# Kernel optimization log

Measured on AMD Instinct MI355X. Metric: run time of the kernel, lower is better.

The kernel has to match this reference:

```python
import jax, jax.numpy as jnp
import numpy as np

N_NODES = 40000
N_EDGES = 640000
D = 128
N_CLASSES = 40
N_GRAPHS = 128


def setup_inputs() -> dict:
    key = jax.random.key(0)
    ks = jax.random.split(key, 8)
    feat = jax.random.normal(ks[0], (N_NODES, D), dtype=jnp.float32)
    s = 1.0 / np.sqrt(D)
    W1 = jax.random.normal(ks[1], (D, D), dtype=jnp.float32) * s
    b1 = jnp.zeros((D,), dtype=jnp.float32)
    W2 = jax.random.normal(ks[2], (D, D), dtype=jnp.float32) * s
    b2 = jnp.zeros((D,), dtype=jnp.float32)
    Wc = jax.random.normal(ks[3], (D, N_CLASSES), dtype=jnp.float32) * s
    bc = jnp.zeros((N_CLASSES,), dtype=jnp.float32)
    src = jax.random.randint(ks[4], (N_EDGES,), 0, N_NODES, dtype=jnp.int32)
    dst = jax.random.randint(ks[5], (N_EDGES,), 0, N_NODES, dtype=jnp.int32)
    graph_ids = jnp.sort(jax.random.randint(ks[6], (N_ODES := N_NODES,), 0, N_GRAPHS, dtype=jnp.int32))
    return {"feat": feat, "W1": W1, "b1": b1, "W2": W2, "b2": b2,
            "Wc": Wc, "bc": bc, "src": src, "dst": dst, "graph_ids": graph_ids}


def _graph_conv(h, W, b, src, dst, norm_src, norm_dst):
    # DGL GraphConv, norm='both': D_in^{-1/2} A D_out^{-1/2} (h W) + b
    h = (h * norm_src[:, None]) @ W                      # [N, D_out]
    agg = jax.ops.segment_sum(h[src], dst, num_segments=N_NODES)  # SpMM gather-scatter
    return agg * norm_dst[:, None] + b


def reference(feat, W1, b1, W2, b2, Wc, bc, src, dst, graph_ids):
    ones_e = jnp.ones((N_EDGES,), dtype=jnp.float32)
    deg_out = jax.ops.segment_sum(ones_e, src, num_segments=N_NODES)
    deg_in = jax.ops.segment_sum(ones_e, dst, num_segments=N_NODES)
    norm_src = jnp.clip(deg_out, 1.0) ** -0.5
    norm_dst = jnp.clip(deg_in, 1.0) ** -0.5

    h = jax.nn.relu(_graph_conv(feat, W1, b1, src, dst, norm_src, norm_dst))
    h = _graph_conv(h, W2, b2, src, dst, norm_src, norm_dst)

    # dgl.mean_nodes: per-graph mean of node features
    sums = jax.ops.segment_sum(h, graph_ids, num_segments=N_GRAPHS)   # [G, D]
    cnts = jax.ops.segment_sum(jnp.ones((N_NODES,), jnp.float32), graph_ids,
                               num_segments=N_GRAPHS)
    hg = sums / jnp.clip(cnts, 1.0)[:, None]
    return hg @ Wc + bc
```

## Files before the change

kernel.cpp:

```cpp
#include <hip/hip_runtime.h>
#include <hip/hip_fp16.h>

#define N_NODES   40000
#define N_EDGES   640000
#define D         128
#define N_CLASSES 40
#define N_GRAPHS  128

#define SCAN_CHUNK 2048
#define SCAN_NB    ((N_NODES + SCAN_CHUNK - 1) / SCAN_CHUNK)

#define NB_H    128
#define CHUNK_H (N_EDGES / NB_H)
#define NWORDS  (N_NODES / 2)
#define DS_NB   ((NWORDS + 255) / 256)

#define SP2_NPW   5

typedef unsigned int uint;
typedef unsigned short u16;
typedef _Float16 f16x8 __attribute__((ext_vector_type(8)));
typedef float f32x4 __attribute__((ext_vector_type(4)));

__global__ __launch_bounds__(1024) void k_histfuse(const int* __restrict__ src,
                                                   const int* __restrict__ dst,
                                                   uint* __restrict__ cntS,
                                                   uint* __restrict__ cntD,
                                                   const float* __restrict__ W2,
                                                   const float* __restrict__ b2,
                                                   const float* __restrict__ Wc,
                                                   float* __restrict__ Wfused,
                                                   float* __restrict__ bfused,
                                                   float* __restrict__ sums,
                                                   uint* __restrict__ blksum) {
    __shared__ uint h[NWORDS];
    const int bg = blockIdx.x, t = threadIdx.x;
    if (bg >= 2 * NB_H) {
        const int k = bg - 2 * NB_H;
        if (k < N_GRAPHS && t < D) sums[k * D + t] = 0.f;
        if (k == 0 && t < 32) blksum[t] = 0;
        if (t < N_CLASSES) {
            const float* row = (k < D) ? &W2[k * D] : b2;
            float s = 0.f;
            #pragma unroll 8
            for (int j = 0; j < D; ++j) s += row[j] * Wc[j * N_CLASSES + t];
            if (k < D) Wfused[k * N_CLASSES + t] = s;
            else bfused[t] = s;
        }
        return;
    }
    const int b = (bg < NB_H) ? bg : bg - NB_H;
    const int* __restrict__ idx = (bg < NB_H) ? src : dst;
    uint* __restrict__ cnt = (bg < NB_H) ? cntS : cntD;
    for (int i = t; i < NWORDS; i += 1024) h[i] = 0;
    __syncthreads();
    const int base = b * CHUNK_H;
    for (int e = t; e < CHUNK_H; e += 1024) {
        int v = idx[base + e];
        atomicAdd(&h[v >> 1], 1u << ((v & 1) * 16));
    }
    __syncthreads();
    for (int i = t; i < NWORDS; i += 1024) cnt[(size_t)b * NWORDS + i] = h[i];
}

__global__ __launch_bounds__(256) void k_degsum(const uint* __restrict__ cntS,
                                                const uint* __restrict__ cntD,
                                                uint* __restrict__ deg_out,
                                                uint* __restrict__ deg_in,
                                                uint* __restrict__ blksum) {
    __shared__ uint wsum[4];
    const int t = threadIdx.x;
    const int w = blockIdx.x * 256 + t;
    uint tot = 0;
    if (w < NWORDS) {
        uint s0 = 0, s1 = 0, d0 = 0, d1 = 0;
        for (int bb = 0; bb < NB_H; ++bb) {
            uint cs = cntS[(size_t)bb * NWORDS + w];
            s0 += cs & 0xffffu; s1 += cs >> 16;
        }
        for (int bb = 0; bb < NB_H; ++bb) {
            uint cd = cntD[(size_t)bb * NWORDS + w];
            d0 += cd & 0xffffu; d1 += cd >> 16;
        }
        deg_out[2 * w] = s0; deg_out[2 * w + 1] = s1;
        deg_in[2 * w]  = d0; deg_in[2 * w + 1]  = d1;
        tot = d0 + d1;
    }
    #pragma unroll
    for (int off = 32; off > 0; off >>= 1) tot += __shfl_down(tot, off);
    if ((t & 63) == 0) wsum[t >> 6] = tot;
    __syncthreads();
    if (t == 0) atomicAdd(&blksum[blockIdx.x >> 2], wsum[0] + wsum[1] + wsum[2] + wsum[3]);
}

__global__ __launch_bounds__(256, 1) void k_scangemm(const uint* __restrict__ deg_in,
                                                     const uint* __restrict__ blksum,
                                                     uint* __restrict__ offsets,
                                                     const int* __restrict__ gid,
                                                     int* __restrict__ bounds,
                                                     const float* __restrict__ feat,
                                                     const float* __restrict__ W1,
                                                     const uint* __restrict__ deg_out,
                                                     __half* __restrict__ hW) {
    __shared__ uint wsum[4];
    const int t = threadIdx.x;
    if (blockIdx.x < SCAN_NB) {
        const int b = blockIdx.x;
        const int lane = t & 63, wave = t >> 6;
        uint basesum = 0;
        for (int q = 0; q < b; ++q) basesum += blksum[q];
        const int base = b * SCAN_CHUNK + t * 8;
        uint v[8];
        uint s = 0;
        #pragma unroll
        for (int j = 0; j < 8; ++j) {
            int idx = base + j;
            v[j] = (idx < N_NODES) ? deg_in[idx] : 0u;
            s += v[j];
        }
        uint inc = s;
        #pragma unroll
        for (int off = 1; off < 64; off <<= 1) {
            uint o = __shfl_up(inc, off);
            if (lane >= off) inc += o;
        }
        if (lane == 63) wsum[wave] = inc;
        __syncthreads();
        if (t < 4) {
            uint w = wsum[t];
            #pragma unroll
            for (int off = 1; off < 4; off <<= 1) {
                uint o = __shfl_up(w, off);
                if (t >= off) w += o;
            }
            wsum[t] = w;
        }
        __syncthreads();
        uint excl = inc - s + (wave ? wsum[wave - 1] : 0u) + basesum;
        #pragma unroll
        for (int j = 0; j < 8; ++j) {
            int idx = base + j;
            if (idx < N_NODES) offsets[idx] = excl;
            excl += v[j];
        }
        if (b == SCAN_NB - 1 && t == 255) offsets[N_NODES] = excl;
        for (int j = 0; j < 8; ++j) {
            int idx = base + j;
            if (idx >= N_NODES) break;
            int g = gid[idx];
            if (idx == 0) {
                for (int q = 0; q <= g; ++q) bounds[q] = 0;
            } else {
                int gp = gid[idx - 1];
                for (int q = gp + 1; q <= g; ++q) bounds[q] = idx;
            }
            if (idx == N_NODES - 1) {
                for (int q = g + 1; q <= N_GRAPHS; ++q) bounds[q] = N_NODES;
            }
        }
        return;
    }
    const int wv = t >> 6, l = t & 63;
    const int kg = l >> 4;
    const int c  = l & 15;
    const int r0 = (blockIdx.x - SCAN_NB) * 64 + wv * 16;

    f16x8 B[4][8];
    #pragma unroll
    for (int ks = 0; ks < 4; ++ks) {
        #pragma unroll
        for (int nt = 0; nt < 8; ++nt) {
            const int kb = ks * 32 + kg * 8;
            const int col = nt * 16 + c;
            f16x8 b;
            #pragma unroll
            for (int i = 0; i < 8; ++i)
                b[i] = (_Float16)W1[(kb + i) * D + col];
            B[ks][nt] = b;
        }
    }

    f32x4 acc[8];
    #pragma unroll
    for (int nt = 0; nt < 8; ++nt) acc[nt] = (f32x4){0.f, 0.f, 0.f, 0.f};

    const int arow = r0 + c;
    #pragma unroll
    for (int ks = 0; ks < 4; ++ks) {
        const float4 q0 = *(const float4*)&feat[(size_t)arow * D + ks * 32 + kg * 8];
        const float4 q1 = *(const float4*)&feat[(size_t)arow * D + ks * 32 + kg * 8 + 4];
        f16x8 a;
        a[0] = (_Float16)q0.x; a[1] = (_Float16)q0.y;
        a[2] = (_Float16)q0.z; a[3] = (_Float16)q0.w;
        a[4] = (_Float16)q1.x; a[5] = (_Float16)q1.y;
        a[6] = (_Float16)q1.z; a[7] = (_Float16)q1.w;
        #pragma unroll
        for (int nt = 0; nt < 8; ++nt)
            acc[nt] = __builtin_amdgcn_mfma_f32_16x16x32_f16(a, B[ks][nt], acc[nt], 0, 0, 0);
    }

    const int rloc = kg * 4;
    float ns[4];
    #pragma unroll
    for (int r = 0; r < 4; ++r)
        ns[r] = rsqrtf(fmaxf((float)deg_out[r0 + rloc + r], 1.f));
    #pragma unroll
    for (int nt = 0; nt < 8; ++nt) {
        #pragma unroll
        for (int r = 0; r < 4; ++r)
            hW[(size_t)(r0 + rloc + r) * D + nt * 16 + c] =
                __float2half(acc[nt][r] * ns[r]);
    }
}

__global__ void k_base(const uint* __restrict__ cntD, u16* __restrict__ baseDelta) {
    int i = blockIdx.x * blockDim.x + threadIdx.x;
    if (i >= N_NODES) return;
    uint run = 0;
    for (int b = 0; b < NB_H; ++b) {
        baseDelta[(size_t)b * N_NODES + i] = (u16)run;
        run += (cntD[(size_t)b * NWORDS + (i >> 1)] >> ((i & 1) * 16)) & 0xffffu;
    }
}

__global__ __launch_bounds__(1024) void k_place(const int* __restrict__ src,
                                                const int* __restrict__ dst,
                                                const uint* __restrict__ offsets,
                                                const u16* __restrict__ baseDelta,
                                                int* __restrict__ csr) {
    __shared__ uint rk[NWORDS];
    const int b = blockIdx.x, t = threadIdx.x;
    for (int i = t; i < NWORDS; i += 1024) rk[i] = 0;
    __syncthreads();
    const int base = b * CHUNK_H;
    for (int e = t; e < CHUNK_H; e += 1024) {
        int d = dst[base + e];
        uint sh = (d & 1) * 16;
        uint old = atomicAdd(&rk[d >> 1], 1u << sh);
        uint r = (old >> sh) & 0xffffu;
        csr[offsets[d] + baseDelta[(size_t)b * N_NODES + d] + r] = src[base + e];
    }
}

__global__ __launch_bounds__(256) void k_spmm1(const __half* __restrict__ X,
                                               const int* __restrict__ csr_src,
                                               const uint* __restrict__ offsets,
                                               const uint* __restrict__ deg_out,
                                               const uint* __restrict__ deg_in,
                                               const float* __restrict__ b1,
                                               __half2* __restrict__ outp) {
    const int lane = threadIdx.x & 63;
    const __half2* __restrict__ Xr = (const __half2*)X;
    int gw = (blockIdx.x * blockDim.x + threadIdx.x) >> 6;
    int nw = (gridDim.x * blockDim.x) >> 6;
    for (int i = gw; i < N_NODES; i += nw) {
        uint e = offsets[i], e1 = offsets[i + 1];
        float2 acc = {0.f, 0.f};
        for (; e + 4 <= e1; e += 4) {
            int s0 = csr_src[e], s1 = csr_src[e + 1];
            int s2 = csr_src[e + 2], s3 = csr_src[e + 3];
            float2 v0 = __half22float2(Xr[(size_t)s0 * 64 + lane]);
            float2 v1 = __half22float2(Xr[(size_t)s1 * 64 + lane]);
            float2 v2 = __half22float2(Xr[(size_t)s2 * 64 + lane]);
            float2 v3 = __half22float2(Xr[(size_t)s3 * 64 + lane]);
            acc.x += (v0.x + v1.x) + (v2.x + v3.x);
            acc.y += (v0.y + v1.y) + (v2.y + v3.y);
        }
        for (; e < e1; ++e) {
            int s = csr_src[e];
            float2 v = __half22float2(Xr[(size_t)s * 64 + lane]);
            acc.x += v.x; acc.y += v.y;
        }
        float nd = rsqrtf(fmaxf((float)deg_in[i], 1.f));
        float ns = rsqrtf(fmaxf((float)deg_out[i], 1.f));
        float2 b = *(const float2*)&b1[lane * 2];
        float rx = fmaxf(acc.x * nd + b.x, 0.f) * ns;
        float ry = fmaxf(acc.y * nd + b.y, 0.f) * ns;
        outp[(size_t)i * 64 + lane] = __floats2half2_rn(rx, ry);
    }
}

__global__ __launch_bounds__(256) void k_spmm2pool(const __half* __restrict__ X,
                                                   const int* __restrict__ csr_src,
                                                   const uint* __restrict__ offsets,
                                                   const uint* __restrict__ deg_in,
                                                   const int* __restrict__ gid,
                                                   float* __restrict__ sums) {
    const int lane = threadIdx.x & 63;
    const int w = (blockIdx.x * blockDim.x + threadIdx.x) >> 6;
    int n0 = w * SP2_NPW;
    if (n0 >= N_NODES) return;
    int n1 = n0 + SP2_NPW; if (n1 > N_NODES) n1 = N_NODES;
    const __half2* __restrict__ Xr = (const __half2*)X;
    float2 seg = {0.f, 0.f};
    int cur = gid[n0];
    for (int i = n0; i < n1; ++i) {
        int g = gid[i];
        if (g != cur) {
            atomicAdd(&sums[cur * D + 2 * lane], seg.x);
            atomicAdd(&sums[cur * D + 2 * lane + 1], seg.y);
            seg.x = 0.f; seg.y = 0.f; cur = g;
        }
        uint e = offsets[i], e1 = offsets[i + 1];
        float2 acc = {0.f, 0.f};
        for (; e + 4 <= e1; e += 4) {
            int s0 = csr_src[e], s1 = csr_src[e + 1];
            int s2 = csr_src[e + 2], s3 = csr_src[e + 3];
            float2 v0 = __half22float2(Xr[(size_t)s0 * 64 + lane]);
            float2 v1 = __half22float2(Xr[(size_t)s1 * 64 + lane]);
            float2 v2 = __half22float2(Xr[(size_t)s2 * 64 + lane]);
            float2 v3 = __half22float2(Xr[(size_t)s3 * 64 + lane]);
            acc.x += (v0.x + v1.x) + (v2.x + v3.x);
            acc.y += (v0.y + v1.y) + (v2.y + v3.y);
        }
        for (; e < e1; ++e) {
            int s = csr_src[e];
            float2 v = __half22float2(Xr[(size_t)s * 64 + lane]);
            acc.x += v.x; acc.y += v.y;
        }
        float nd = rsqrtf(fmaxf((float)deg_in[i], 1.f));
        seg.x += acc.x * nd;
        seg.y += acc.y * nd;
    }
    atomicAdd(&sums[cur * D + 2 * lane], seg.x);
    atomicAdd(&sums[cur * D + 2 * lane + 1], seg.y);
}

__global__ __launch_bounds__(64) void k_out(const float* __restrict__ sums,
                                            const int* __restrict__ bounds,
                                            const float* __restrict__ Wfused,
                                            const float* __restrict__ bfused,
                                            const float* __restrict__ bc,
                                            float* __restrict__ out) {
    int g = blockIdx.x, c = threadIdx.x;
    if (c >= N_CLASSES) return;
    int cnt = bounds[g + 1] - bounds[g];
    float inv = (cnt > 0) ? 1.f / (float)cnt : 0.f;
    float s = 0.f;
    #pragma unroll 8
    for (int k = 0; k < D; ++k) s += sums[g * D + k] * Wfused[k * N_CLASSES + c];
    out[g * N_CLASSES + c] = s * inv + (cnt > 0 ? bfused[c] : 0.f) + bc[c];
}

extern "C" void kernel_launch(void* const* d_in, const int* in_sizes, int n_in,
                              void* d_out, int out_size, void* d_ws, size_t ws_size,
                              hipStream_t stream) {
    const float* feat = (const float*)d_in[0];
    const float* W1   = (const float*)d_in[1];
    const float* b1   = (const float*)d_in[2];
    const float* W2   = (const float*)d_in[3];
    const float* b2   = (const float*)d_in[4];
    const float* Wc   = (const float*)d_in[5];
    const float* bc   = (const float*)d_in[6];
    const int*   src  = (const int*)d_in[7];
    const int*   dst  = (const int*)d_in[8];
    const int*   gid  = (const int*)d_in[9];
    float* out = (float*)d_out;

    char* w = (char*)d_ws;
    uint* deg_out = (uint*)w; w += (size_t)N_NODES * 4;
    uint* deg_in  = (uint*)w; w += (size_t)N_NODES * 4;
    uint* offsets = (uint*)w; w += (size_t)(N_NODES + 4) * 4;
    int*  bounds  = (int*)w;  w += 132 * 4;
    uint* blksum  = (uint*)w; w += 32 * 4;
    float* Wfused = (float*)w; w += (size_t)D * N_CLASSES * 4;
    float* bfused = (float*)w; w += 64 * 4;
    float* sums   = (float*)w; w += (size_t)N_GRAPHS * D * 4;
    char* regA = w; w += (size_t)NB_H * NWORDS * 4;
    uint* cntS  = (uint*)regA;
    int*  csr   = (int*)regA;
    char* regB = w; w += (size_t)NB_H * NWORDS * 4;
    uint* cntD  = (uint*)regB;
    __half* h1s = (__half*)regB;
    u16* baseDelta = (u16*)w; w += (size_t)NB_H * N_NODES * 2;
    __half* hW  = (__half*)w; w += (size_t)N_NODES * D * 2;

    k_histfuse<<<2 * NB_H + D + 1, 1024, 0, stream>>>(src, dst, cntS, cntD,
                                                      W2, b2, Wc, Wfused, bfused,
                                                      sums, blksum);
    k_degsum<<<DS_NB, 256, 0, stream>>>(cntS, cntD, deg_out, deg_in, blksum);
    k_scangemm<<<SCAN_NB + 625, 256, 0, stream>>>(deg_in, blksum, offsets, gid, bounds,
                                                  feat, W1, deg_out, hW);
    k_base<<<(N_NODES + 255) / 256, 256, 0, stream>>>(cntD, baseDelta);
    k_place<<<NB_H, 1024, 0, stream>>>(src, dst, offsets, baseDelta, csr);
    k_spmm1<<<2048, 256, 0, stream>>>(hW, csr, offsets, deg_out, deg_in, b1, (__half2*)h1s);
    k_spmm2pool<<<2048, 256, 0, stream>>>(h1s, csr, offsets, deg_in, gid, sums);
    k_out<<<N_GRAPHS, 64, 0, stream>>>(sums, bounds, Wfused, bfused, bc, out);
}
```

Before: 149.6 us.

## Store layer-1 activations in FP8 and merge base-delta kernel into degree sum

The intermediate layer-1 output is now packed as two FP8 values per 16-bit word instead of half2, which halves the bytes gathered per edge in the second SpMM-plus-pool kernel. Separately, the per-block base-delta prefix computation is folded into the degree-sum kernel as extra blocks, removing one launch and letting it run alongside the degree reduction. FP8 storage lowers the precision of the hidden activations, which risks accuracy against the reference.

Measured after the change: 134.9 us. -9.8%, faster.

```diff
diff --git a/kernel.cpp b/kernel.cpp
--- a/kernel.cpp
+++ b/kernel.cpp
@@ -14,6 +14,7 @@
 #define CHUNK_H (N_EDGES / NB_H)
 #define NWORDS  (N_NODES / 2)
 #define DS_NB   ((NWORDS + 255) / 256)
+#define BASE_NB ((N_NODES + 255) / 256)
 
 #define SP2_NPW   5
 
@@ -21,6 +22,7 @@
 typedef unsigned short u16;
 typedef _Float16 f16x8 __attribute__((ext_vector_type(8)));
 typedef float f32x4 __attribute__((ext_vector_type(4)));
+typedef float f32x2 __attribute__((ext_vector_type(2)));
 
 __global__ __launch_bounds__(1024) void k_histfuse(const int* __restrict__ src,
                                                    const int* __restrict__ dst,
@@ -63,34 +65,46 @@
     for (int i = t; i < NWORDS; i += 1024) cnt[(size_t)b * NWORDS + i] = h[i];
 }
 
-__global__ __launch_bounds__(256) void k_degsum(const uint* __restrict__ cntS,
-                                                const uint* __restrict__ cntD,
-                                                uint* __restrict__ deg_out,
-                                                uint* __restrict__ deg_in,
-                                                uint* __restrict__ blksum) {
+__global__ __launch_bounds__(256) void k_degbase(const uint* __restrict__ cntS,
+                                                 const uint* __restrict__ cntD,
+                                                 uint* __restrict__ deg_out,
+                                                 uint* __restrict__ deg_in,
+                                                 uint* __restrict__ blksum,
+                                                 u16* __restrict__ baseDelta) {
     __shared__ uint wsum[4];
     const int t = threadIdx.x;
-    const int w = blockIdx.x * 256 + t;
-    uint tot = 0;
-    if (w < NWORDS) {
-        uint s0 = 0, s1 = 0, d0 = 0, d1 = 0;
-        for (int bb = 0; bb < NB_H; ++bb) {
-            uint cs = cntS[(size_t)bb * NWORDS + w];
-            s0 += cs & 0xffffu; s1 += cs >> 16;
-        }
-        for (int bb = 0; bb < NB_H; ++bb) {
-            uint cd = cntD[(size_t)bb * NWORDS + w];
-            d0 += cd & 0xffffu; d1 += cd >> 16;
-        }
-        deg_out[2 * w] = s0; deg_out[2 * w + 1] = s1;
-        deg_in[2 * w]  = d0; deg_in[2 * w + 1]  = d1;
-        tot = d0 + d1;
-    }
-    #pragma unroll
-    for (int off = 32; off > 0; off >>= 1) tot += __shfl_down(tot, off);
-    if ((t & 63) == 0) wsum[t >> 6] = tot;
-    __syncthreads();
-    if (t == 0) atomicAdd(&blksum[blockIdx.x >> 2], wsum[0] + wsum[1] + wsum[2] + wsum[3]);
+    if (blockIdx.x < DS_NB) {
+        const int w = blockIdx.x * 256 + t;
+        uint tot = 0;
+        if (w < NWORDS) {
+            uint s0 = 0, s1 = 0, d0 = 0, d1 = 0;
+            for (int bb = 0; bb < NB_H; ++bb) {
+                uint cs = cntS[(size_t)bb * NWORDS + w];
+                s0 += cs & 0xffffu; s1 += cs >> 16;
+            }
+            for (int bb = 0; bb < NB_H; ++bb) {
+                uint cd = cntD[(size_t)bb * NWORDS + w];
+                d0 += cd & 0xffffu; d1 += cd >> 16;
+            }
+            deg_out[2 * w] = s0; deg_out[2 * w + 1] = s1;
+            deg_in[2 * w]  = d0; deg_in[2 * w + 1]  = d1;
+            tot = d0 + d1;
+        }
+        #pragma unroll
+        for (int off = 32; off > 0; off >>= 1) tot += __shfl_down(tot, off);
+        if ((t & 63) == 0) wsum[t >> 6] = tot;
+        __syncthreads();
+        if (t == 0) atomicAdd(&blksum[blockIdx.x >> 2],
+                              wsum[0] + wsum[1] + wsum[2] + wsum[3]);
+        return;
+    }
+    int i = (blockIdx.x - DS_NB) * 256 + t;
+    if (i >= N_NODES) return;
+    uint run = 0;
+    for (int b = 0; b < NB_H; ++b) {
+        baseDelta[(size_t)b * N_NODES + i] = (u16)run;
+        run += (cntD[(size_t)b * NWORDS + (i >> 1)] >> ((i & 1) * 16)) & 0xffffu;
+    }
 }
 
 __global__ __launch_bounds__(256, 1) void k_scangemm(const uint* __restrict__ deg_in,
@@ -213,16 +227,6 @@
     }
 }
 
-__global__ void k_base(const uint* __restrict__ cntD, u16* __restrict__ baseDelta) {
-    int i = blockIdx.x * blockDim.x + threadIdx.x;
-    if (i >= N_NODES) return;
-    uint run = 0;
-    for (int b = 0; b < NB_H; ++b) {
-        baseDelta[(size_t)b * N_NODES + i] = (u16)run;
-        run += (cntD[(size_t)b * NWORDS + (i >> 1)] >> ((i & 1) * 16)) & 0xffffu;
-    }
-}
-
 __global__ __launch_bounds__(1024) void k_place(const int* __restrict__ src,
                                                 const int* __restrict__ dst,
                                                 const uint* __restrict__ offsets,
@@ -248,7 +252,7 @@
                                                const uint* __restrict__ deg_out,
                                                const uint* __restrict__ deg_in,
                                                const float* __restrict__ b1,
-                                               __half2* __restrict__ outp) {
+                                               ushort* __restrict__ outp) {
     const int lane = threadIdx.x & 63;
     const __half2* __restrict__ Xr = (const __half2*)X;
     int gw = (blockIdx.x * blockDim.x + threadIdx.x) >> 6;
@@ -276,11 +280,12 @@
         float2 b = *(const float2*)&b1[lane * 2];
         float rx = fmaxf(acc.x * nd + b.x, 0.f) * ns;
         float ry = fmaxf(acc.y * nd + b.y, 0.f) * ns;
-        outp[(size_t)i * 64 + lane] = __floats2half2_rn(rx, ry);
-    }
-}
-
-__global__ __launch_bounds__(256) void k_spmm2pool(const __half* __restrict__ X,
+        int pk = __builtin_amdgcn_cvt_pk_fp8_f32(rx, ry, 0, false);
+        outp[(size_t)i * 64 + lane] = (ushort)pk;
+    }
+}
+
+__global__ __launch_bounds__(256) void k_spmm2pool(const ushort* __restrict__ X16,
                                                    const int* __restrict__ csr_src,
                                                    const uint* __restrict__ offsets,
                                                    const uint* __restrict__ deg_in,
@@ -291,39 +296,36 @@
     int n0 = w * SP2_NPW;
     if (n0 >= N_NODES) return;
     int n1 = n0 + SP2_NPW; if (n1 > N_NODES) n1 = N_NODES;
-    const __half2* __restrict__ Xr = (const __half2*)X;
-    float2 seg = {0.f, 0.f};
+    f32x2 seg = {0.f, 0.f};
     int cur = gid[n0];
     for (int i = n0; i < n1; ++i) {
         int g = gid[i];
         if (g != cur) {
-            atomicAdd(&sums[cur * D + 2 * lane], seg.x);
-            atomicAdd(&sums[cur * D + 2 * lane + 1], seg.y);
-            seg.x = 0.f; seg.y = 0.f; cur = g;
+            atomicAdd(&sums[cur * D + 2 * lane], seg[0]);
+            atomicAdd(&sums[cur * D + 2 * lane + 1], seg[1]);
+            seg[0] = 0.f; seg[1] = 0.f; cur = g;
         }
         uint e = offsets[i], e1 = offsets[i + 1];
-        float2 acc = {0.f, 0.f};
+        f32x2 acc = {0.f, 0.f};
         for (; e + 4 <= e1; e += 4) {
             int s0 = csr_src[e], s1 = csr_src[e + 1];
             int s2 = csr_src[e + 2], s3 = csr_src[e + 3];
-            float2 v0 = __half22float2(Xr[(size_t)s0 * 64 + lane]);
-            float2 v1 = __half22float2(Xr[(size_t)s1 * 64 + lane]);
-            float2 v2 = __half22float2(Xr[(size_t)s2 * 64 + lane]);
-            float2 v3 = __half22float2(Xr[(size_t)s3 * 64 + lane]);
-            acc.x += (v0.x + v1.x) + (v2.x + v3.x);
-            acc.y += (v0.y + v1.y) + (v2.y + v3.y);
+            f32x2 v0 = __builtin_amdgcn_cvt_pk_f32_fp8(X16[(size_t)s0 * 64 + lane], false);
+            f32x2 v1 = __builtin_amdgcn_cvt_pk_f32_fp8(X16[(size_t)s1 * 64 + lane], false);
+            f32x2 v2 = __builtin_amdgcn_cvt_pk_f32_fp8(X16[(size_t)s2 * 64 + lane], false);
+            f32x2 v3 = __builtin_amdgcn_cvt_pk_f32_fp8(X16[(size_t)s3 * 64 + lane], false);
+            acc += (v0 + v1) + (v2 + v3);
         }
         for (; e < e1; ++e) {
             int s = csr_src[e];
-            float2 v = __half22float2(Xr[(size_t)s * 64 + lane]);
-            acc.x += v.x; acc.y += v.y;
+            acc += __builtin_amdgcn_cvt_pk_f32_fp8(X16[(size_t)s * 64 + lane], false);
         }
         float nd = rsqrtf(fmaxf((float)deg_in[i], 1.f));
-        seg.x += acc.x * nd;
-        seg.y += acc.y * nd;
-    }
-    atomicAdd(&sums[cur * D + 2 * lane], seg.x);
-    atomicAdd(&sums[cur * D + 2 * lane + 1], seg.y);
+        seg[0] += acc[0] * nd;
+        seg[1] += acc[1] * nd;
+    }
+    atomicAdd(&sums[cur * D + 2 * lane], seg[0]);
+    atomicAdd(&sums[cur * D + 2 * lane + 1], seg[1]);
 }
 
 __global__ __launch_bounds__(64) void k_out(const float* __restrict__ sums,
@@ -371,19 +373,19 @@
     int*  csr   = (int*)regA;
     char* regB = w; w += (size_t)NB_H * NWORDS * 4;
     uint* cntD  = (uint*)regB;
-    __half* h1s = (__half*)regB;
+    ushort* h1s = (ushort*)regB;
     u16* baseDelta = (u16*)w; w += (size_t)NB_H * N_NODES * 2;
     __half* hW  = (__half*)w; w += (size_t)N_NODES * D * 2;
 
     k_histfuse<<<2 * NB_H + D + 1, 1024, 0, stream>>>(src, dst, cntS, cntD,
                                                       W2, b2, Wc, Wfused, bfused,
                                                       sums, blksum);
-    k_degsum<<<DS_NB, 256, 0, stream>>>(cntS, cntD, deg_out, deg_in, blksum);
+    k_degbase<<<DS_NB + BASE_NB, 256, 0, stream>>>(cntS, cntD, deg_out, deg_in,
+                                                   blksum, baseDelta);
     k_scangemm<<<SCAN_NB + 625, 256, 0, stream>>>(deg_in, blksum, offsets, gid, bounds,
                                                   feat, W1, deg_out, hW);
-    k_base<<<(N_NODES + 255) / 256, 256, 0, stream>>>(cntD, baseDelta);
     k_place<<<NB_H, 1024, 0, stream>>>(src, dst, offsets, baseDelta, csr);
-    k_spmm1<<<2048, 256, 0, stream>>>(hW, csr, offsets, deg_out, deg_in, b1, (__half2*)h1s);
+    k_spmm1<<<2048, 256, 0, stream>>>(hW, csr, offsets, deg_out, deg_in, b1, h1s);
     k_spmm2pool<<<2048, 256, 0, stream>>>(h1s, csr, offsets, deg_in, gid, sums);
     k_out<<<N_GRAPHS, 64, 0, stream>>>(sums, bounds, Wfused, bfused, bc, out);
 }
```
